# Performance work log

Hardware: AMD Instinct MI355X
Metric: run time of the kernel (lower is better)

## Reference

```python
import jax, jax.numpy as jnp
import numpy as np

B, N, FD, H = 8, 256, 1024, 256
RATIO, TEMP = 0.6, 0.5


def setup_inputs() -> dict:
    key = jax.random.key(0)
    ks = jax.random.split(key, 5)
    x = jax.random.normal(ks[0], (B, N, FD), dtype=jnp.float32)
    s1 = 1.0 / np.sqrt(2 * FD)
    W1 = jax.random.uniform(ks[1], (H, 2 * FD), minval=-s1, maxval=s1, dtype=jnp.float32)
    b1 = jax.random.uniform(ks[2], (H,), minval=-s1, maxval=s1, dtype=jnp.float32)
    s2 = 1.0 / np.sqrt(H)
    W2 = jax.random.uniform(ks[3], (1, H), minval=-s2, maxval=s2, dtype=jnp.float32)
    b2 = jax.random.uniform(ks[4], (1,), minval=-s2, maxval=s2, dtype=jnp.float32)
    return {"x": x, "W1": W1, "b1": b1, "W2": W2, "b2": b2}


def reference(x, W1, b1, W2, b2):
    Bb, Nn, Fd = x.shape
    # Linear on cat([row, col]) == row @ W1[:, :F].T + col @ W1[:, F:].T + b1,
    # so project nodes once and broadcast-add instead of materializing [N,N,2F].
    pr = jnp.einsum('bnf,hf->bnh', x, W1[:, :Fd])  # row projections
    pc = jnp.einsum('bnf,hf->bnh', x, W1[:, Fd:])  # col projections
    h = jax.nn.relu(pr[:, :, None, :] + pc[:, None, :, :] + b1)  # [B,N,N,H]
    edge_scores = jnp.einsum('bijh,h->bij', h, W2[0]) + b2[0]    # [B,N,N]
    flat = edge_scores.reshape(Bb, Nn * Nn)
    soft_mask = jax.nn.softmax(flat / TEMP, axis=1)
    k = int(RATIO * Nn * Nn)
    topk_vals, _ = jax.lax.top_k(soft_mask, k)
    threshold = topk_vals[:, -1:]
    causal_mask = jnp.where(soft_mask >= threshold, soft_mask, jnp.zeros_like(soft_mask))
    causal_mask = causal_mask / (causal_mask.sum(axis=1, keepdims=True) + 1e-12)
    conf_mask = 1.0 - causal_mask
    causal_adj = causal_mask.reshape(Bb, Nn, Nn)
    conf_adj = conf_mask.reshape(Bb, Nn, Nn)
    return (causal_adj, conf_adj, edge_scores, soft_mask)
```

## Files before the change

### kernel.cpp

```cpp
#include <hip/hip_runtime.h>

#define BB 8
#define NN 256
#define FDIM 1024
#define HDIM 256
#define NSQ 65536
#define ROWS 2048
#define KSEL 39321
#define NBIN 8192

typedef short s16x8 __attribute__((ext_vector_type(8)));
typedef float f32x4 __attribute__((ext_vector_type(4)));

__device__ __forceinline__ unsigned fkey(float f) {
  unsigned u = __float_as_uint(f);
  return (u & 0x80000000u) ? ~u : (u | 0x80000000u);
}
__device__ __forceinline__ float finv(unsigned k) {
  unsigned u = (k & 0x80000000u) ? (k & 0x7fffffffu) : ~k;
  return __uint_as_float(u);
}
__device__ __forceinline__ unsigned short f2bf(float f) {
  unsigned u = __float_as_uint(f);
  unsigned r = (u + 0x7fffu + ((u >> 16) & 1u)) >> 16;
  return (unsigned short)r;
}

__global__ __launch_bounds__(256) void k_prep(const float* __restrict__ X,
                                              const float* __restrict__ W1,
                                              unsigned short* __restrict__ XB,
                                              unsigned short* __restrict__ W1B,
                                              unsigned* __restrict__ zero) {
  const int bx = blockIdx.x, t = threadIdx.x;
  if (bx < 1280) {
    const float* src = (bx < 1024) ? X : W1;
    unsigned short* dst = (bx < 1024) ? XB : W1B;
    const int idx = ((bx < 1024 ? bx : bx - 1024) * 256 + t) * 8;
    float4 v0 = *(const float4*)&src[idx];
    float4 v1 = *(const float4*)&src[idx + 4];
    s16x8 o;
    o[0] = (short)f2bf(v0.x); o[1] = (short)f2bf(v0.y); o[2] = (short)f2bf(v0.z); o[3] = (short)f2bf(v0.w);
    o[4] = (short)f2bf(v1.x); o[5] = (short)f2bf(v1.y); o[6] = (short)f2bf(v1.z); o[7] = (short)f2bf(v1.w);
    *(s16x8*)&dst[idx] = o;
  } else {
    const int idx = ((bx - 1280) * 256 + t) * 4;
    *(uint4*)&zero[idx] = make_uint4(0u, 0u, 0u, 0u);
  }
}

#define LDSW 72
__global__ __launch_bounds__(256) void k_gemm(const unsigned short* __restrict__ XB,
                                              const unsigned short* __restrict__ W1B,
                                              const float* __restrict__ b1,
                                              float* __restrict__ PRBT,
                                              float* __restrict__ PCT) {
  const int bm = blockIdx.x * 64;
  const int bn = blockIdx.y * 64;
  const int t = threadIdx.x;
  __shared__ short As[64 * LDSW];
  __shared__ short Bs[64 * LDSW];
  const int sr = t >> 2, cg = t & 3;
  const unsigned short* pa = XB + (bm + sr) * FDIM + cg * 16;
  const unsigned short* pb = (bn < 256)
      ? (W1B + (bn + sr) * (2 * FDIM) + cg * 16)
      : (W1B + (bn - 256 + sr) * (2 * FDIM) + FDIM + cg * 16);
  const int w = t >> 6, lane = t & 63;
  const int wm = (w >> 1) * 32, wn = (w & 1) * 32;
  const int q = lane >> 4, m16 = lane & 15;
  f32x4 acc[2][2] = {};
  s16x8 ra0 = *(const s16x8*)(pa);
  s16x8 ra1 = *(const s16x8*)(pa + 8);
  s16x8 rb0 = *(const s16x8*)(pb);
  s16x8 rb1 = *(const s16x8*)(pb + 8);
  for (int k0 = 0; k0 < FDIM; k0 += 64) {
    __syncthreads();
    *(s16x8*)&As[sr * LDSW + cg * 16]     = ra0;
    *(s16x8*)&As[sr * LDSW + cg * 16 + 8] = ra1;
    *(s16x8*)&Bs[sr * LDSW + cg * 16]     = rb0;
    *(s16x8*)&Bs[sr * LDSW + cg * 16 + 8] = rb1;
    if (k0 + 64 < FDIM) {
      ra0 = *(const s16x8*)(pa + k0 + 64);
      ra1 = *(const s16x8*)(pa + k0 + 72);
      rb0 = *(const s16x8*)(pb + k0 + 64);
      rb1 = *(const s16x8*)(pb + k0 + 72);
    }
    __syncthreads();
    {
      s16x8 af0 = *(s16x8*)&As[(wm + m16) * LDSW + q * 8];
      s16x8 af1 = *(s16x8*)&As[(wm + 16 + m16) * LDSW + q * 8];
      s16x8 bf0 = *(s16x8*)&Bs[(wn + m16) * LDSW + q * 8];
      s16x8 bf1 = *(s16x8*)&Bs[(wn + 16 + m16) * LDSW + q * 8];
      acc[0][0] = __builtin_amdgcn_mfma_f32_16x16x32_bf16(af0, bf0, acc[0][0], 0, 0, 0);
      acc[0][1] = __builtin_amdgcn_mfma_f32_16x16x32_bf16(af0, bf1, acc[0][1], 0, 0, 0);
      acc[1][0] = __builtin_amdgcn_mfma_f32_16x16x32_bf16(af1, bf0, acc[1][0], 0, 0, 0);
      acc[1][1] = __builtin_amdgcn_mfma_f32_16x16x32_bf16(af1, bf1, acc[1][1], 0, 0, 0);
    }
    {
      s16x8 af0 = *(s16x8*)&As[(wm + m16) * LDSW + 32 + q * 8];
      s16x8 af1 = *(s16x8*)&As[(wm + 16 + m16) * LDSW + 32 + q * 8];
      s16x8 bf0 = *(s16x8*)&Bs[(wn + m16) * LDSW + 32 + q * 8];
      s16x8 bf1 = *(s16x8*)&Bs[(wn + 16 + m16) * LDSW + 32 + q * 8];
      acc[0][0] = __builtin_amdgcn_mfma_f32_16x16x32_bf16(af0, bf0, acc[0][0], 0, 0, 0);
      acc[0][1] = __builtin_amdgcn_mfma_f32_16x16x32_bf16(af0, bf1, acc[0][1], 0, 0, 0);
      acc[1][0] = __builtin_amdgcn_mfma_f32_16x16x32_bf16(af1, bf0, acc[1][0], 0, 0, 0);
      acc[1][1] = __builtin_amdgcn_mfma_f32_16x16x32_bf16(af1, bf1, acc[1][1], 0, 0, 0);
    }
  }
#pragma unroll
  for (int rt = 0; rt < 2; ++rt) {
#pragma unroll
    for (int ct = 0; ct < 2; ++ct) {
      const int hn = bn + wn + ct * 16 + m16;
      const int row0 = bm + wm + rt * 16 + q * 4;
      if (hn < 256) {
        const float bias = b1[hn];
        float4 v = make_float4(acc[rt][ct][0] + bias, acc[rt][ct][1] + bias,
                               acc[rt][ct][2] + bias, acc[rt][ct][3] + bias);
        *(float4*)&PRBT[hn * ROWS + row0] = v;
      } else {
        float4 v = make_float4(acc[rt][ct][0], acc[rt][ct][1],
                               acc[rt][ct][2], acc[rt][ct][3]);
        *(float4*)&PCT[(hn - 256) * ROWS + row0] = v;
      }
    }
  }
}

__global__ __launch_bounds__(512) void k_edge(const float* __restrict__ PRBT,
                                              const float* __restrict__ PCT,
                                              const float* __restrict__ W2,
                                              const float* __restrict__ b2,
                                              float* __restrict__ edge,
                                              unsigned* __restrict__ gcount,
                                              float* __restrict__ gvsum) {
  const int b = blockIdx.z;
  const int i0 = blockIdx.y * 64, j0 = blockIdx.x * 32;
  const int t = threadIdx.x;
  __shared__ float prs[64][68];
  __shared__ float pcs[64][36];
  __shared__ float w2s[HDIM];
  __shared__ unsigned lhc[NBIN / 2];
  __shared__ float lhv[NBIN];
  if (t < HDIM) w2s[t] = W2[t];
#pragma unroll
  for (int i = 0; i < 2; ++i) ((uint4*)lhc)[t + i * 512] = make_uint4(0u, 0u, 0u, 0u);
#pragma unroll
  for (int i = 0; i < 4; ++i) ((float4*)lhv)[t + i * 512] = make_float4(0.f, 0.f, 0.f, 0.f);
  const float bias = b2[0];
  const int tmi = t >> 4, tnj = t & 15;
  float acc[2][2] = {};
  for (int h0 = 0; h0 < HDIM; h0 += 64) {
    __syncthreads();
#pragma unroll
    for (int s = 0; s < 2; ++s) {
      int idx = t + s * 512;
      int hh = idx >> 4, ig = idx & 15;
      *(float4*)&prs[hh][ig * 4] =
          *(const float4*)&PRBT[(h0 + hh) * ROWS + b * NN + i0 + ig * 4];
    }
    {
      int hh = t >> 3, jg = t & 7;
      *(float4*)&pcs[hh][jg * 4] =
          *(const float4*)&PCT[(h0 + hh) * ROWS + b * NN + j0 + jg * 4];
    }
    __syncthreads();
#pragma unroll 8
    for (int h = 0; h < 64; ++h) {
      const float w = w2s[h0 + h];
      const float2 a = *(const float2*)&prs[h][tmi * 2];
      const float2 c = *(const float2*)&pcs[h][tnj * 2];
      acc[0][0] += fmaxf(a.x + c.x, 0.f) * w;
      acc[0][1] += fmaxf(a.x + c.y, 0.f) * w;
      acc[1][0] += fmaxf(a.y + c.x, 0.f) * w;
      acc[1][1] += fmaxf(a.y + c.y, 0.f) * w;
    }
  }
  const int ibase = i0 + tmi * 2, jbase = j0 + tnj * 2;
#pragma unroll
  for (int i = 0; i < 2; ++i) {
    float2 v = make_float2(acc[i][0] + bias, acc[i][1] + bias);
    *(float2*)&edge[b * NSQ + (ibase + i) * NN + jbase] = v;
    float ex = __expf(v.x * 2.f), ey = __expf(v.y * 2.f);
    unsigned bx = fkey(v.x) >> 19, by = fkey(v.y) >> 19;
    atomicAdd(&lhc[bx >> 1], 1u << ((bx & 1) * 16));
    atomicAdd(&lhv[bx], ex);
    atomicAdd(&lhc[by >> 1], 1u << ((by & 1) * 16));
    atomicAdd(&lhv[by], ey);
  }
  __syncthreads();
  unsigned* gc = gcount + b * NBIN;
  float* gv = gvsum + b * NBIN;
#pragma unroll
  for (int i = 0; i < 8; ++i) {
    const int idx = t + i * 512;
    unsigned wv = lhc[idx];
    if (wv) {
      unsigned lo = wv & 0xFFFFu, hi = wv >> 16;
      if (lo) atomicAdd(&gc[2 * idx], lo);
      if (hi) atomicAdd(&gc[2 * idx + 1], hi);
    }
  }
#pragma unroll
  for (int i = 0; i < 16; ++i) {
    const int idx = t + i * 512;
    float vv = lhv[idx];
    if (vv != 0.f) atomicAdd(&gv[idx], vv);
  }
}

__global__ __launch_bounds__(256) void k_out(const float* __restrict__ edge,
                                             const unsigned* __restrict__ gcount,
                                             const float* __restrict__ gvsum,
                                             float* __restrict__ soft,
                                             float* __restrict__ causal,
                                             float* __restrict__ conf) {
  const int b = blockIdx.y;
  const int t = threadIdx.x;
  __shared__ unsigned S[256];
  __shared__ float V[256];
  __shared__ unsigned ou[1];
  __shared__ float of[3];
  const unsigned* hc = gcount + b * NBIN;
  const float* hv = gvsum + b * NBIN;
  unsigned cs = 0; float vs = 0.f;
  for (int i = 0; i < 32; ++i) { cs += hc[t * 32 + i]; vs += hv[t * 32 + i]; }
  S[t] = cs; V[t] = vs;
  __syncthreads();
  for (int off = 1; off < 256; off <<= 1) {
    unsigned su = (t + off < 256) ? S[t + off] : 0u;
    float vu = (t + off < 256) ? V[t + off] : 0.f;
    __syncthreads();
    S[t] += su; V[t] += vu;
    __syncthreads();
  }
  if (t == 0) of[2] = V[0];
  const int above = (int)(S[t] - cs);
  if (above < KSEL && (int)S[t] >= KSEL) {
    int cum = above;
    float vcum = V[t] - vs;
    for (int i = 31; i >= 0; --i) {
      unsigned c = hc[t * 32 + i];
      float v = hv[t * 32 + i];
      cum += (int)c;
      if (cum >= KSEL) { ou[0] = (unsigned)(t * 32 + i); of[0] = vcum; of[1] = v; break; }
      vcum += v;
    }
  }
  __syncthreads();
  const float th = finv(ou[0] << 19);
  const float Z = of[2];
  const float invZ = 1.f / Z;
  const float msum = (of[0] + of[1]) * invZ;
  const float invD = 1.f / (msum + 1e-12f);
  const int off = b * NSQ + blockIdx.x * 2048 + t * 8;
#pragma unroll
  for (int i = 0; i < 8; i += 4) {
    float4 v = *(const float4*)&edge[off + i];
    float4 o = make_float4(__expf(v.x * 2.f) * invZ, __expf(v.y * 2.f) * invZ,
                           __expf(v.z * 2.f) * invZ, __expf(v.w * 2.f) * invZ);
    *(float4*)&soft[off + i] = o;
    float cx = v.x >= th ? o.x * invD : 0.f;
    float cy = v.y >= th ? o.y * invD : 0.f;
    float cz = v.z >= th ? o.z * invD : 0.f;
    float cw = v.w >= th ? o.w * invD : 0.f;
    *(float4*)&causal[off + i] = make_float4(cx, cy, cz, cw);
    *(float4*)&conf[off + i]   = make_float4(1.f - cx, 1.f - cy, 1.f - cz, 1.f - cw);
  }
}

extern "C" void kernel_launch(void* const* d_in, const int* in_sizes, int n_in,
                              void* d_out, int out_size, void* d_ws, size_t ws_size,
                              hipStream_t stream) {
  const float* x  = (const float*)d_in[0];
  const float* W1 = (const float*)d_in[1];
  const float* b1 = (const float*)d_in[2];
  const float* W2 = (const float*)d_in[3];
  const float* b2 = (const float*)d_in[4];

  float* out = (float*)d_out;
  float* causal = out;
  float* conf   = out + 1 * 524288;
  float* edge   = out + 2 * 524288;
  float* soft   = out + 3 * 524288;

  float* ws = (float*)d_ws;
  float*          PRBT   = ws;
  float*          PCT    = ws + 524288;
  unsigned short* XB     = (unsigned short*)(ws + 1048576);
  unsigned short* W1B    = (unsigned short*)(ws + 2097152);
  unsigned*       gcount = (unsigned*)(ws + 2359296);
  float*          gvsum  = (float*)(ws + 2424832);

  k_prep<<<1408, 256, 0, stream>>>(x, W1, XB, W1B, gcount);
  k_gemm<<<dim3(32, 8), 256, 0, stream>>>(XB, W1B, b1, PRBT, PCT);
  k_edge<<<dim3(8, 4, 8), 512, 0, stream>>>(PRBT, PCT, W2, b2, edge, gcount, gvsum);
  k_out<<<dim3(32, 8), 256, 0, stream>>>(edge, gcount, gvsum, soft, causal, conf);
}
```

Before: 106.5 us.

## Fuse four kernels into one cooperative kernel with grid syncs

Replaces the prep, GEMM, edge-score and output kernels with a single cooperative kernel of 256 blocks of 512 threads, separated by grid.sync barriers. The edge values are kept in registers across the histogram phase, so the final softmax and mask pass no longer re-reads the edge array from global memory. The GEMM tile mapping is reworked for 8 waves per block. The cost is three grid-wide barriers, lower parallelism in the conversion and GEMM phases, and a dependency on all blocks being co-resident.

```diff
diff --git a/kernel.cpp b/kernel.cpp
--- a/kernel.cpp
+++ b/kernel.cpp
@@ -1,4 +1,7 @@
 #include <hip/hip_runtime.h>
+#include <hip/hip_cooperative_groups.h>
+
+namespace cg = cooperative_groups;
 
 #define BB 8
 #define NN 256
@@ -8,6 +11,7 @@
 #define ROWS 2048
 #define KSEL 39321
 #define NBIN 8192
+#define LDSW 72
 
 typedef short s16x8 __attribute__((ext_vector_type(8)));
 typedef float f32x4 __attribute__((ext_vector_type(4)));
@@ -26,245 +30,231 @@
   return (unsigned short)r;
 }
 
-__global__ __launch_bounds__(256) void k_prep(const float* __restrict__ X,
-                                              const float* __restrict__ W1,
-                                              unsigned short* __restrict__ XB,
-                                              unsigned short* __restrict__ W1B,
-                                              unsigned* __restrict__ zero) {
+__global__ __launch_bounds__(512, 2) void k_fused(
+    const float* __restrict__ X, const float* __restrict__ W1,
+    const float* __restrict__ b1, const float* __restrict__ W2,
+    const float* __restrict__ b2,
+    unsigned short* __restrict__ XB, unsigned short* __restrict__ W1B,
+    float* __restrict__ PRBT, float* __restrict__ PCT,
+    float* __restrict__ edge, unsigned* __restrict__ gcount,
+    float* __restrict__ gvsum, float* __restrict__ soft,
+    float* __restrict__ causal, float* __restrict__ conf) {
+  __shared__ __align__(16) char smem[76800];
+  cg::grid_group grid = cg::this_grid();
   const int bx = blockIdx.x, t = threadIdx.x;
-  if (bx < 1280) {
-    const float* src = (bx < 1024) ? X : W1;
-    unsigned short* dst = (bx < 1024) ? XB : W1B;
-    const int idx = ((bx < 1024 ? bx : bx - 1024) * 256 + t) * 8;
-    float4 v0 = *(const float4*)&src[idx];
-    float4 v1 = *(const float4*)&src[idx + 4];
-    s16x8 o;
-    o[0] = (short)f2bf(v0.x); o[1] = (short)f2bf(v0.y); o[2] = (short)f2bf(v0.z); o[3] = (short)f2bf(v0.w);
-    o[4] = (short)f2bf(v1.x); o[5] = (short)f2bf(v1.y); o[6] = (short)f2bf(v1.z); o[7] = (short)f2bf(v1.w);
-    *(s16x8*)&dst[idx] = o;
-  } else {
-    const int idx = ((bx - 1280) * 256 + t) * 4;
-    *(uint4*)&zero[idx] = make_uint4(0u, 0u, 0u, 0u);
-  }
-}
-
-#define LDSW 72
-__global__ __launch_bounds__(256) void k_gemm(const unsigned short* __restrict__ XB,
-                                              const unsigned short* __restrict__ W1B,
-                                              const float* __restrict__ b1,
-                                              float* __restrict__ PRBT,
-                                              float* __restrict__ PCT) {
-  const int bm = blockIdx.x * 64;
-  const int bn = blockIdx.y * 64;
-  const int t = threadIdx.x;
-  __shared__ short As[64 * LDSW];
-  __shared__ short Bs[64 * LDSW];
-  const int sr = t >> 2, cg = t & 3;
-  const unsigned short* pa = XB + (bm + sr) * FDIM + cg * 16;
-  const unsigned short* pb = (bn < 256)
-      ? (W1B + (bn + sr) * (2 * FDIM) + cg * 16)
-      : (W1B + (bn - 256 + sr) * (2 * FDIM) + FDIM + cg * 16);
-  const int w = t >> 6, lane = t & 63;
-  const int wm = (w >> 1) * 32, wn = (w & 1) * 32;
-  const int q = lane >> 4, m16 = lane & 15;
-  f32x4 acc[2][2] = {};
-  s16x8 ra0 = *(const s16x8*)(pa);
-  s16x8 ra1 = *(const s16x8*)(pa + 8);
-  s16x8 rb0 = *(const s16x8*)(pb);
-  s16x8 rb1 = *(const s16x8*)(pb + 8);
-  for (int k0 = 0; k0 < FDIM; k0 += 64) {
-    __syncthreads();
-    *(s16x8*)&As[sr * LDSW + cg * 16]     = ra0;
-    *(s16x8*)&As[sr * LDSW + cg * 16 + 8] = ra1;
-    *(s16x8*)&Bs[sr * LDSW + cg * 16]     = rb0;
-    *(s16x8*)&Bs[sr * LDSW + cg * 16 + 8] = rb1;
-    if (k0 + 64 < FDIM) {
-      ra0 = *(const s16x8*)(pa + k0 + 64);
-      ra1 = *(const s16x8*)(pa + k0 + 72);
-      rb0 = *(const s16x8*)(pb + k0 + 64);
-      rb1 = *(const s16x8*)(pb + k0 + 72);
-    }
-    __syncthreads();
+
+  {
+    const int g = bx * 512 + t;
     {
-      s16x8 af0 = *(s16x8*)&As[(wm + m16) * LDSW + q * 8];
-      s16x8 af1 = *(s16x8*)&As[(wm + 16 + m16) * LDSW + q * 8];
-      s16x8 bf0 = *(s16x8*)&Bs[(wn + m16) * LDSW + q * 8];
-      s16x8 bf1 = *(s16x8*)&Bs[(wn + 16 + m16) * LDSW + q * 8];
-      acc[0][0] = __builtin_amdgcn_mfma_f32_16x16x32_bf16(af0, bf0, acc[0][0], 0, 0, 0);
-      acc[0][1] = __builtin_amdgcn_mfma_f32_16x16x32_bf16(af0, bf1, acc[0][1], 0, 0, 0);
-      acc[1][0] = __builtin_amdgcn_mfma_f32_16x16x32_bf16(af1, bf0, acc[1][0], 0, 0, 0);
-      acc[1][1] = __builtin_amdgcn_mfma_f32_16x16x32_bf16(af1, bf1, acc[1][1], 0, 0, 0);
-    }
-    {
-      s16x8 af0 = *(s16x8*)&As[(wm + m16) * LDSW + 32 + q * 8];
-      s16x8 af1 = *(s16x8*)&As[(wm + 16 + m16) * LDSW + 32 + q * 8];
-      s16x8 bf0 = *(s16x8*)&Bs[(wn + m16) * LDSW + 32 + q * 8];
-      s16x8 bf1 = *(s16x8*)&Bs[(wn + 16 + m16) * LDSW + 32 + q * 8];
-      acc[0][0] = __builtin_amdgcn_mfma_f32_16x16x32_bf16(af0, bf0, acc[0][0], 0, 0, 0);
-      acc[0][1] = __builtin_amdgcn_mfma_f32_16x16x32_bf16(af0, bf1, acc[0][1], 0, 0, 0);
-      acc[1][0] = __builtin_amdgcn_mfma_f32_16x16x32_bf16(af1, bf0, acc[1][0], 0, 0, 0);
-      acc[1][1] = __builtin_amdgcn_mfma_f32_16x16x32_bf16(af1, bf1, acc[1][1], 0, 0, 0);
-    }
-  }
-#pragma unroll
-  for (int rt = 0; rt < 2; ++rt) {
+      const int i16 = g * 16;
+      float4 v0 = *(const float4*)&X[i16];
+      float4 v1 = *(const float4*)&X[i16 + 4];
+      float4 v2 = *(const float4*)&X[i16 + 8];
+      float4 v3 = *(const float4*)&X[i16 + 12];
+      s16x8 o0, o1;
+      o0[0] = (short)f2bf(v0.x); o0[1] = (short)f2bf(v0.y); o0[2] = (short)f2bf(v0.z); o0[3] = (short)f2bf(v0.w);
+      o0[4] = (short)f2bf(v1.x); o0[5] = (short)f2bf(v1.y); o0[6] = (short)f2bf(v1.z); o0[7] = (short)f2bf(v1.w);
+      o1[0] = (short)f2bf(v2.x); o1[1] = (short)f2bf(v2.y); o1[2] = (short)f2bf(v2.z); o1[3] = (short)f2bf(v2.w);
+      o1[4] = (short)f2bf(v3.x); o1[5] = (short)f2bf(v3.y); o1[6] = (short)f2bf(v3.z); o1[7] = (short)f2bf(v3.w);
+      *(s16x8*)&XB[i16] = o0;
+      *(s16x8*)&XB[i16 + 8] = o1;
+    }
+    if (g < 32768) {
+      const int i16 = g * 16;
+      float4 v0 = *(const float4*)&W1[i16];
+      float4 v1 = *(const float4*)&W1[i16 + 4];
+      float4 v2 = *(const float4*)&W1[i16 + 8];
+      float4 v3 = *(const float4*)&W1[i16 + 12];
+      s16x8 o0, o1;
+      o0[0] = (short)f2bf(v0.x); o0[1] = (short)f2bf(v0.y); o0[2] = (short)f2bf(v0.z); o0[3] = (short)f2bf(v0.w);
+      o0[4] = (short)f2bf(v1.x); o0[5] = (short)f2bf(v1.y); o0[6] = (short)f2bf(v1.z); o0[7] = (short)f2bf(v1.w);
+      o1[0] = (short)f2bf(v2.x); o1[1] = (short)f2bf(v2.y); o1[2] = (short)f2bf(v2.z); o1[3] = (short)f2bf(v2.w);
+      o1[4] = (short)f2bf(v3.x); o1[5] = (short)f2bf(v3.y); o1[6] = (short)f2bf(v3.z); o1[7] = (short)f2bf(v3.w);
+      *(s16x8*)&W1B[i16] = o0;
+      *(s16x8*)&W1B[i16 + 8] = o1;
+      ((uint4*)gcount)[g] = make_uint4(0u, 0u, 0u, 0u);
+    }
+  }
+  grid.sync();
+
+  {
+    short* As = (short*)smem;
+    short* Bs = As + 64 * LDSW;
+    const int bm = (bx & 31) * 64;
+    const int bn = (bx >> 5) * 64;
+    const int srow = t >> 3, scg = t & 7;
+    const unsigned short* pa = XB + (bm + srow) * FDIM + scg * 8;
+    const unsigned short* pb = (bn < 256)
+        ? (W1B + (bn + srow) * (2 * FDIM) + scg * 8)
+        : (W1B + (bn - 256 + srow) * (2 * FDIM) + FDIM + scg * 8);
+    const int w = t >> 6, lane = t & 63;
+    const int wr = (w & 3) * 16;
+    const int wc = (w >> 2) * 32;
+    const int q = lane >> 4, m16 = lane & 15;
+    f32x4 acc[2] = {};
+    s16x8 ra = *(const s16x8*)(pa);
+    s16x8 rb = *(const s16x8*)(pb);
+    for (int k0 = 0; k0 < FDIM; k0 += 64) {
+      __syncthreads();
+      *(s16x8*)&As[srow * LDSW + scg * 8] = ra;
+      *(s16x8*)&Bs[srow * LDSW + scg * 8] = rb;
+      if (k0 + 64 < FDIM) {
+        ra = *(const s16x8*)(pa + k0 + 64);
+        rb = *(const s16x8*)(pb + k0 + 64);
+      }
+      __syncthreads();
+#pragma unroll
+      for (int koff = 0; koff < 64; koff += 32) {
+        s16x8 af  = *(s16x8*)&As[(wr + m16) * LDSW + koff + q * 8];
+        s16x8 bf0 = *(s16x8*)&Bs[(wc + m16) * LDSW + koff + q * 8];
+        s16x8 bf1 = *(s16x8*)&Bs[(wc + 16 + m16) * LDSW + koff + q * 8];
+        acc[0] = __builtin_amdgcn_mfma_f32_16x16x32_bf16(af, bf0, acc[0], 0, 0, 0);
+        acc[1] = __builtin_amdgcn_mfma_f32_16x16x32_bf16(af, bf1, acc[1], 0, 0, 0);
+      }
+    }
 #pragma unroll
     for (int ct = 0; ct < 2; ++ct) {
-      const int hn = bn + wn + ct * 16 + m16;
-      const int row0 = bm + wm + rt * 16 + q * 4;
+      const int hn = bn + wc + ct * 16 + m16;
+      const int row0 = bm + wr + q * 4;
       if (hn < 256) {
         const float bias = b1[hn];
-        float4 v = make_float4(acc[rt][ct][0] + bias, acc[rt][ct][1] + bias,
-                               acc[rt][ct][2] + bias, acc[rt][ct][3] + bias);
+        float4 v = make_float4(acc[ct][0] + bias, acc[ct][1] + bias,
+                               acc[ct][2] + bias, acc[ct][3] + bias);
         *(float4*)&PRBT[hn * ROWS + row0] = v;
       } else {
-        float4 v = make_float4(acc[rt][ct][0], acc[rt][ct][1],
-                               acc[rt][ct][2], acc[rt][ct][3]);
+        float4 v = make_float4(acc[ct][0], acc[ct][1], acc[ct][2], acc[ct][3]);
         *(float4*)&PCT[(hn - 256) * ROWS + row0] = v;
       }
     }
   }
-}
-
-__global__ __launch_bounds__(512) void k_edge(const float* __restrict__ PRBT,
-                                              const float* __restrict__ PCT,
-                                              const float* __restrict__ W2,
-                                              const float* __restrict__ b2,
-                                              float* __restrict__ edge,
-                                              unsigned* __restrict__ gcount,
-                                              float* __restrict__ gvsum) {
-  const int b = blockIdx.z;
-  const int i0 = blockIdx.y * 64, j0 = blockIdx.x * 32;
-  const int t = threadIdx.x;
-  __shared__ float prs[64][68];
-  __shared__ float pcs[64][36];
-  __shared__ float w2s[HDIM];
-  __shared__ unsigned lhc[NBIN / 2];
-  __shared__ float lhv[NBIN];
-  if (t < HDIM) w2s[t] = W2[t];
-#pragma unroll
-  for (int i = 0; i < 2; ++i) ((uint4*)lhc)[t + i * 512] = make_uint4(0u, 0u, 0u, 0u);
-#pragma unroll
-  for (int i = 0; i < 4; ++i) ((float4*)lhv)[t + i * 512] = make_float4(0.f, 0.f, 0.f, 0.f);
-  const float bias = b2[0];
+  grid.sync();
+
+  float (*prs)[68] = (float(*)[68])smem;
+  float (*pcs)[36] = (float(*)[36])(smem + 17408);
+  float* w2s       = (float*)(smem + 26624);
+  unsigned* lhc    = (unsigned*)(smem + 27648);
+  float* lhv       = (float*)(smem + 44032);
+  const int b = bx >> 5;
+  const int i0 = ((bx >> 3) & 3) * 64, j0 = (bx & 7) * 32;
   const int tmi = t >> 4, tnj = t & 15;
-  float acc[2][2] = {};
-  for (int h0 = 0; h0 < HDIM; h0 += 64) {
+  const int ibase = i0 + tmi * 2, jbase = j0 + tnj * 2;
+  float2 ev[2];
+  {
+    if (t < HDIM) w2s[t] = W2[t];
+#pragma unroll
+    for (int i = 0; i < 2; ++i) ((uint4*)lhc)[t + i * 512] = make_uint4(0u, 0u, 0u, 0u);
+#pragma unroll
+    for (int i = 0; i < 4; ++i) ((float4*)lhv)[t + i * 512] = make_float4(0.f, 0.f, 0.f, 0.f);
+    const float bias = b2[0];
+    float acc[2][2] = {};
+    for (int h0 = 0; h0 < HDIM; h0 += 64) {
+      __syncthreads();
+#pragma unroll
+      for (int s = 0; s < 2; ++s) {
+        int idx = t + s * 512;
+        int hh = idx >> 4, ig = idx & 15;
+        *(float4*)&prs[hh][ig * 4] =
+            *(const float4*)&PRBT[(h0 + hh) * ROWS + b * NN + i0 + ig * 4];
+      }
+      {
+        int hh = t >> 3, jg = t & 7;
+        *(float4*)&pcs[hh][jg * 4] =
+            *(const float4*)&PCT[(h0 + hh) * ROWS + b * NN + j0 + jg * 4];
+      }
+      __syncthreads();
+#pragma unroll 8
+      for (int h = 0; h < 64; ++h) {
+        const float w = w2s[h0 + h];
+        const float2 a = *(const float2*)&prs[h][tmi * 2];
+        const float2 c = *(const float2*)&pcs[h][tnj * 2];
+        acc[0][0] += fmaxf(a.x + c.x, 0.f) * w;
+        acc[0][1] += fmaxf(a.x + c.y, 0.f) * w;
+        acc[1][0] += fmaxf(a.y + c.x, 0.f) * w;
+        acc[1][1] += fmaxf(a.y + c.y, 0.f) * w;
+      }
+    }
+#pragma unroll
+    for (int i = 0; i < 2; ++i) {
+      float2 v = make_float2(acc[i][0] + bias, acc[i][1] + bias);
+      ev[i] = v;
+      *(float2*)&edge[b * NSQ + (ibase + i) * NN + jbase] = v;
+      float ex = __expf(v.x * 2.f), ey = __expf(v.y * 2.f);
+      unsigned bxk = fkey(v.x) >> 19, byk = fkey(v.y) >> 19;
+      atomicAdd(&lhc[bxk >> 1], 1u << ((bxk & 1) * 16));
+      atomicAdd(&lhv[bxk], ex);
+      atomicAdd(&lhc[byk >> 1], 1u << ((byk & 1) * 16));
+      atomicAdd(&lhv[byk], ey);
+    }
     __syncthreads();
-#pragma unroll
-    for (int s = 0; s < 2; ++s) {
-      int idx = t + s * 512;
-      int hh = idx >> 4, ig = idx & 15;
-      *(float4*)&prs[hh][ig * 4] =
-          *(const float4*)&PRBT[(h0 + hh) * ROWS + b * NN + i0 + ig * 4];
-    }
-    {
-      int hh = t >> 3, jg = t & 7;
-      *(float4*)&pcs[hh][jg * 4] =
-          *(const float4*)&PCT[(h0 + hh) * ROWS + b * NN + j0 + jg * 4];
-    }
+    unsigned* gc = gcount + b * NBIN;
+    float* gv = gvsum + b * NBIN;
+#pragma unroll
+    for (int i = 0; i < 8; ++i) {
+      const int idx = t + i * 512;
+      unsigned wv = lhc[idx];
+      if (wv) {
+        unsigned lo = wv & 0xFFFFu, hi = wv >> 16;
+        if (lo) atomicAdd(&gc[2 * idx], lo);
+        if (hi) atomicAdd(&gc[2 * idx + 1], hi);
+      }
+    }
+#pragma unroll
+    for (int i = 0; i < 16; ++i) {
+      const int idx = t + i * 512;
+      float vv = lhv[idx];
+      if (vv != 0.f) atomicAdd(&gv[idx], vv);
+    }
+  }
+  grid.sync();
+
+  {
+    unsigned* S = (unsigned*)smem;
+    float* V    = (float*)(smem + 2048);
+    unsigned* ou = (unsigned*)(smem + 4096);
+    float* of    = (float*)(smem + 4112);
+    const unsigned* hc = gcount + b * NBIN;
+    const float* hv = gvsum + b * NBIN;
+    unsigned cs = 0; float vs = 0.f;
+#pragma unroll
+    for (int i = 0; i < 16; ++i) { cs += hc[t * 16 + i]; vs += hv[t * 16 + i]; }
+    S[t] = cs; V[t] = vs;
     __syncthreads();
-#pragma unroll 8
-    for (int h = 0; h < 64; ++h) {
-      const float w = w2s[h0 + h];
-      const float2 a = *(const float2*)&prs[h][tmi * 2];
-      const float2 c = *(const float2*)&pcs[h][tnj * 2];
-      acc[0][0] += fmaxf(a.x + c.x, 0.f) * w;
-      acc[0][1] += fmaxf(a.x + c.y, 0.f) * w;
-      acc[1][0] += fmaxf(a.y + c.x, 0.f) * w;
-      acc[1][1] += fmaxf(a.y + c.y, 0.f) * w;
-    }
-  }
-  const int ibase = i0 + tmi * 2, jbase = j0 + tnj * 2;
-#pragma unroll
-  for (int i = 0; i < 2; ++i) {
-    float2 v = make_float2(acc[i][0] + bias, acc[i][1] + bias);
-    *(float2*)&edge[b * NSQ + (ibase + i) * NN + jbase] = v;
-    float ex = __expf(v.x * 2.f), ey = __expf(v.y * 2.f);
-    unsigned bx = fkey(v.x) >> 19, by = fkey(v.y) >> 19;
-    atomicAdd(&lhc[bx >> 1], 1u << ((bx & 1) * 16));
-    atomicAdd(&lhv[bx], ex);
-    atomicAdd(&lhc[by >> 1], 1u << ((by & 1) * 16));
-    atomicAdd(&lhv[by], ey);
-  }
-  __syncthreads();
-  unsigned* gc = gcount + b * NBIN;
-  float* gv = gvsum + b * NBIN;
-#pragma unroll
-  for (int i = 0; i < 8; ++i) {
-    const int idx = t + i * 512;
-    unsigned wv = lhc[idx];
-    if (wv) {
-      unsigned lo = wv & 0xFFFFu, hi = wv >> 16;
-      if (lo) atomicAdd(&gc[2 * idx], lo);
-      if (hi) atomicAdd(&gc[2 * idx + 1], hi);
-    }
-  }
-#pragma unroll
-  for (int i = 0; i < 16; ++i) {
-    const int idx = t + i * 512;
-    float vv = lhv[idx];
-    if (vv != 0.f) atomicAdd(&gv[idx], vv);
-  }
-}
-
-__global__ __launch_bounds__(256) void k_out(const float* __restrict__ edge,
-                                             const unsigned* __restrict__ gcount,
-                                             const float* __restrict__ gvsum,
-                                             float* __restrict__ soft,
-                                             float* __restrict__ causal,
-                                             float* __restrict__ conf) {
-  const int b = blockIdx.y;
-  const int t = threadIdx.x;
-  __shared__ unsigned S[256];
-  __shared__ float V[256];
-  __shared__ unsigned ou[1];
-  __shared__ float of[3];
-  const unsigned* hc = gcount + b * NBIN;
-  const float* hv = gvsum + b * NBIN;
-  unsigned cs = 0; float vs = 0.f;
-  for (int i = 0; i < 32; ++i) { cs += hc[t * 32 + i]; vs += hv[t * 32 + i]; }
-  S[t] = cs; V[t] = vs;
-  __syncthreads();
-  for (int off = 1; off < 256; off <<= 1) {
-    unsigned su = (t + off < 256) ? S[t + off] : 0u;
-    float vu = (t + off < 256) ? V[t + off] : 0.f;
+    for (int off = 1; off < 512; off <<= 1) {
+      unsigned su = (t + off < 512) ? S[t + off] : 0u;
+      float vu = (t + off < 512) ? V[t + off] : 0.f;
+      __syncthreads();
+      S[t] += su; V[t] += vu;
+      __syncthreads();
+    }
+    if (t == 0) of[2] = V[0];
+    const int above = (int)(S[t] - cs);
+    if (above < KSEL && (int)S[t] >= KSEL) {
+      int cum = above;
+      float vcum = V[t] - vs;
+      for (int i = 15; i >= 0; --i) {
+        unsigned c = hc[t * 16 + i];
+        float v = hv[t * 16 + i];
+        cum += (int)c;
+        if (cum >= KSEL) { ou[0] = (unsigned)(t * 16 + i); of[0] = vcum; of[1] = v; break; }
+        vcum += v;
+      }
+    }
     __syncthreads();
-    S[t] += su; V[t] += vu;
-    __syncthreads();
-  }
-  if (t == 0) of[2] = V[0];
-  const int above = (int)(S[t] - cs);
-  if (above < KSEL && (int)S[t] >= KSEL) {
-    int cum = above;
-    float vcum = V[t] - vs;
-    for (int i = 31; i >= 0; --i) {
-      unsigned c = hc[t * 32 + i];
-      float v = hv[t * 32 + i];
-      cum += (int)c;
-      if (cum >= KSEL) { ou[0] = (unsigned)(t * 32 + i); of[0] = vcum; of[1] = v; break; }
-      vcum += v;
-    }
-  }
-  __syncthreads();
-  const float th = finv(ou[0] << 19);
-  const float Z = of[2];
-  const float invZ = 1.f / Z;
-  const float msum = (of[0] + of[1]) * invZ;
-  const float invD = 1.f / (msum + 1e-12f);
-  const int off = b * NSQ + blockIdx.x * 2048 + t * 8;
-#pragma unroll
-  for (int i = 0; i < 8; i += 4) {
-    float4 v = *(const float4*)&edge[off + i];
-    float4 o = make_float4(__expf(v.x * 2.f) * invZ, __expf(v.y * 2.f) * invZ,
-                           __expf(v.z * 2.f) * invZ, __expf(v.w * 2.f) * invZ);
-    *(float4*)&soft[off + i] = o;
-    float cx = v.x >= th ? o.x * invD : 0.f;
-    float cy = v.y >= th ? o.y * invD : 0.f;
-    float cz = v.z >= th ? o.z * invD : 0.f;
-    float cw = v.w >= th ? o.w * invD : 0.f;
-    *(float4*)&causal[off + i] = make_float4(cx, cy, cz, cw);
-    *(float4*)&conf[off + i]   = make_float4(1.f - cx, 1.f - cy, 1.f - cz, 1.f - cw);
+    const float th = finv(ou[0] << 19);
+    const float invZ = 1.f / of[2];
+    const float msum = (of[0] + of[1]) * invZ;
+    const float invD = 1.f / (msum + 1e-12f);
+#pragma unroll
+    for (int i = 0; i < 2; ++i) {
+      const float2 v = ev[i];
+      const int pos = b * NSQ + (ibase + i) * NN + jbase;
+      float ox = __expf(v.x * 2.f) * invZ, oy = __expf(v.y * 2.f) * invZ;
+      *(float2*)&soft[pos] = make_float2(ox, oy);
+      float cx = v.x >= th ? ox * invD : 0.f;
+      float cy = v.y >= th ? oy * invD : 0.f;
+      *(float2*)&causal[pos] = make_float2(cx, cy);
+      *(float2*)&conf[pos]   = make_float2(1.f - cx, 1.f - cy);
+    }
   }
 }
 
@@ -291,8 +281,12 @@
   unsigned*       gcount = (unsigned*)(ws + 2359296);
   float*          gvsum  = (float*)(ws + 2424832);
 
-  k_prep<<<1408, 256, 0, stream>>>(x, W1, XB, W1B, gcount);
-  k_gemm<<<dim3(32, 8), 256, 0, stream>>>(XB, W1B, b1, PRBT, PCT);
-  k_edge<<<dim3(8, 4, 8), 512, 0, stream>>>(PRBT, PCT, W2, b2, edge, gcount, gvsum);
-  k_out<<<dim3(32, 8), 256, 0, stream>>>(edge, gcount, gvsum, soft, causal, conf);
-}
+  void* args[] = {
+    (void*)&x, (void*)&W1, (void*)&b1, (void*)&W2, (void*)&b2,
+    (void*)&XB, (void*)&W1B, (void*)&PRBT, (void*)&PCT,
+    (void*)&edge, (void*)&gcount, (void*)&gvsum,
+    (void*)&soft, (void*)&causal, (void*)&conf
+  };
+  hipLaunchCooperativeKernel((const void*)k_fused, dim3(256), dim3(512),
+                             args, 0, stream);
+}
```

New measurement: 208.2 us. 95.5% more time.
